# Optimization experiments

Measured on AMD Instinct MI355X. Metric: run time of the kernel, lower is better.

## Reference

```python
import jax, jax.numpy as jnp
import numpy as np
import math

DIM = 1024
HEADS = 16
WINDOW = 256  # window_size; also used as block size (band covers 3 blocks)


def _rope(x):
    # canonical half-split RoPE over the FULL feature dim (as the module applies
    # it before the head split), base 10000
    b, s, d = x.shape
    half = d // 2
    inv_freq = 1.0 / (10000.0 ** (jnp.arange(half, dtype=jnp.float32) / half))
    ang = jnp.arange(s, dtype=jnp.float32)[:, None] * inv_freq[None, :]  # [s, half]
    cos, sin = jnp.cos(ang), jnp.sin(ang)
    x1, x2 = x[..., :half], x[..., half:]
    return jnp.concatenate([x1 * cos - x2 * sin, x1 * sin + x2 * cos], axis=-1)


def setup_inputs() -> dict:
    key = jax.random.key(0)
    ks = jax.random.split(key, 8)
    d = DIM
    q = jax.random.normal(ks[0], (2, 4096, d), dtype=jnp.float32)
    k = jax.random.normal(ks[1], (2, 4096, d), dtype=jnp.float32)
    v = jax.random.normal(ks[2], (2, 4096, d), dtype=jnp.float32)
    wq = jax.random.normal(ks[3], (d, d), dtype=jnp.float32) * 0.02
    wk = jax.random.normal(ks[4], (d, d), dtype=jnp.float32) * 0.02
    wv = jax.random.normal(ks[5], (d, d), dtype=jnp.float32) * 0.02
    wo_w = jax.random.normal(ks[6], (d, d), dtype=jnp.float32) * 0.02
    wo_b = jnp.zeros((d,), dtype=jnp.float32)
    return {"q": q, "k": k, "v": v, "wq": wq, "wk": wk, "wv": wv,
            "wo_w": wo_w, "wo_b": wo_b}


def reference(q, k, v, wq, wk, wv, wo_w, wo_b):
    b, s, d = q.shape
    h, W = HEADS, WINDOW
    dk = d // h
    B = W                      # block size == window -> band of 3 blocks
    nb = s // B

    # projections (torch Linear: x @ W^T), then RoPE over the full dim
    qp = _rope(jnp.einsum('bsd,ed->bse', q, wq))
    kp = _rope(jnp.einsum('bsd,ed->bse', k, wk))
    vp = jnp.einsum('bsd,ed->bse', v, wv)

    # split heads -> [b, h, s, dk]
    qh = qp.reshape(b, s, h, dk).transpose(0, 2, 1, 3)
    kh = kp.reshape(b, s, h, dk).transpose(0, 2, 1, 3)
    vh = vp.reshape(b, s, h, dk).transpose(0, 2, 1, 3)

    # pad keys/values by one block on each side, gather 3-block bands
    kpad = jnp.pad(kh, ((0, 0), (0, 0), (B, B), (0, 0)))
    vpad = jnp.pad(vh, ((0, 0), (0, 0), (B, B), (0, 0)))
    kblk = kpad.reshape(b, h, nb + 2, B, dk)
    vblk = vpad.reshape(b, h, nb + 2, B, dk)
    kband = jnp.concatenate([kblk[:, :, i:i + nb] for i in range(3)], axis=3)  # [b,h,nb,3B,dk]
    vband = jnp.concatenate([vblk[:, :, i:i + nb] for i in range(3)], axis=3)

    qb = qh.reshape(b, h, nb, B, dk)
    # NOTE: original multiplies by sqrt(dim_k) (not divides) -- kept faithfully
    scores = jnp.einsum('bhnqd,bhnkd->bhnqk', qb, kband) * math.sqrt(dk)

    # band mask: key global pos = (n-1)*B + ki, query global pos = n*B + qi
    n_idx = jnp.arange(nb)[:, None, None]
    qi = jnp.arange(B)[None, :, None]
    ki = jnp.arange(3 * B)[None, None, :]
    kpos = (n_idx - 1) * B + ki
    rel = ki - B - qi  # key_pos - query_pos
    valid = (rel >= -W) & (rel <= W) & (kpos >= 0) & (kpos < s)  # [nb,B,3B]

    neg = jnp.asarray(jnp.finfo(scores.dtype).min, scores.dtype)
    scores = jnp.where(valid[None, None], scores, neg)
    attn = jax.nn.softmax(scores, axis=-1)

    out = jnp.einsum('bhnqk,bhnkd->bhnqd', attn, vband)
    out = out.reshape(b, h, s, dk).transpose(0, 2, 1, 3).reshape(b, s, d)
    return jnp.einsum('bsd,ed->bse', out, wo_w) + wo_b
```

## Files before the change

kernel.cpp:

```cpp
#include <hip/hip_runtime.h>


typedef __attribute__((ext_vector_type(8))) short short8v;
typedef __attribute__((ext_vector_type(4))) float float4v;
typedef __attribute__((ext_vector_type(8))) _Float16 half8v;

#define MFMA_BF16(A_, B_, C_) __builtin_amdgcn_mfma_f32_16x16x32_bf16((A_), (B_), (C_), 0, 0, 0)
#define MFMA_F16(A_, B_, C_)  __builtin_amdgcn_mfma_f32_16x16x32_f16((A_), (B_), (C_), 0, 0, 0)

#define VMW_(n) asm volatile("s_waitcnt vmcnt(" #n ")" ::: "memory")
#define VMW(n) VMW_(n)
#define LGKM0 asm volatile("s_waitcnt lgkmcnt(0)" ::: "memory")
#define BARF do { __builtin_amdgcn_s_barrier(); asm volatile("" ::: "memory"); } while (0)
#define FENCE asm volatile("" ::: "memory")

__device__ __forceinline__ void split_rn(float x, short& h, short& l) {
    unsigned int u = __float_as_uint(x);
    u += 0x7fffu + ((u >> 16) & 1u);
    unsigned int hb = u & 0xffff0000u;
    h = (short)(hb >> 16);
    float lo = x - __uint_as_float(hb);
    l = (short)(__float_as_uint(lo) >> 16);
}

__device__ __forceinline__ void dma16(const void* g, void* l) {
    __builtin_amdgcn_global_load_lds(
        (__attribute__((address_space(1))) void*)g,
        (__attribute__((address_space(3))) void*)l, 16, 0, 0);
}

__global__ __launch_bounds__(256) void prep_k(
    const float* __restrict__ wq, const float* __restrict__ wk,
    const float* __restrict__ wv, unsigned short* __restrict__ scr)
{
    const int M1 = 1 << 20;
    unsigned int tid = blockIdx.x * 256 + threadIdx.x;
    if (tid < (unsigned)M1) {
        short h, l; split_rn(wq[tid], h, l);
        scr[tid] = (unsigned short)h;
        scr[M1 + tid] = (unsigned short)l;
    } else if (tid < (unsigned)(2 * M1)) {
        unsigned int i = tid - M1;
        short h, l; split_rn(wk[i], h, l);
        scr[2 * M1 + i] = (unsigned short)h;
        scr[3 * M1 + i] = (unsigned short)l;
    } else {
        unsigned int i = tid - 2 * M1;
        scr[4 * M1 + i] = __builtin_bit_cast(unsigned short, (_Float16)wv[i]);
    }
}

__global__ __launch_bounds__(512, 2) void gemm_qk2(
    const float* __restrict__ A0, const short* __restrict__ Bh0,
    const short* __restrict__ Bl0, float* __restrict__ C0,
    const float* __restrict__ A1, const short* __restrict__ Bh1,
    const short* __restrict__ Bl1, float* __restrict__ C1)
{
    __shared__ __align__(16) short S[2 * 32768];

    const int bid = blockIdx.x;
    const int cid = ((bid & 7) << 5) | (bid >> 3);
    const int z   = cid >> 7;
    const int rem = cid & 127;
    const int bm  = (rem >> 2) << 8;
    const int bn  = (rem & 3) << 8;

    const float* Ap  = z ? A1  : A0;
    const short* Bhp = z ? Bh1 : Bh0;
    const short* Blp = z ? Bl1 : Bl0;
    float*       Cp  = z ? C1  : C0;

    const int t = threadIdx.x;
    const int wave = t >> 6, lane = t & 63;
    const int c16 = lane & 15, quad = lane >> 4;
    const int wm = (wave >> 2) << 7;
    const int wn = (wave & 3) << 6;

    const int ar = t >> 1;
    const int ah16 = (t & 1) << 4;
    const int fA = (ar & 3) ^ ((ar >> 2) & 3);
    const int swA0 = ((((t & 1) << 1) | 0) ^ fA) << 3;
    const int swA1 = ((((t & 1) << 1) | 1) ^ fA) << 3;

    const int br  = lane >> 2;
    const int fsl = (((lane & 3) ^ ((br & 3) ^ ((br >> 2) & 3))) << 3);

    const int frd = ((quad ^ ((c16 & 3) ^ ((c16 >> 2) & 3))) << 3);

    float4v acc[8][4];
#pragma unroll
    for (int i = 0; i < 8; i++)
#pragma unroll
        for (int j = 0; j < 4; j++) acc[i][j] = (float4v){0.f, 0.f, 0.f, 0.f};

#define STAGE_B(pp, kk)                                                          \
    do {                                                                         \
        const size_t rb = (size_t)(bn + (wave << 5) + br) * 1024 + (kk) + fsl;   \
        short* dh = S + (pp) * 32768 + 16384 + (wave << 10);                     \
        short* dl = dh + 8192;                                                   \
        dma16(Bhp + rb,             dh);                                         \
        dma16(Bhp + rb + 16 * 1024, dh + 512);                                   \
        dma16(Blp + rb,             dl);                                         \
        dma16(Blp + rb + 16 * 1024, dl + 512);                                   \
    } while (0)

#define SPLIT_WRITE(sp_)                                                         \
    do {                                                                         \
        short8v h0, l0, h1, l1;                                                  \
        _Pragma("unroll")                                                        \
        for (int jj = 0; jj < 4; jj++) {                                         \
            short hh, ll;                                                        \
            split_rn(ap0[jj], hh, ll); h0[jj] = hh;     l0[jj] = ll;             \
            split_rn(ap1[jj], hh, ll); h0[jj + 4] = hh; l0[jj + 4] = ll;         \
            split_rn(ap2[jj], hh, ll); h1[jj] = hh;     l1[jj] = ll;             \
            split_rn(ap3[jj], hh, ll); h1[jj + 4] = hh; l1[jj + 4] = ll;         \
        }                                                                        \
        short* abase = (sp_) + ar * 32;                                          \
        *(short8v*)(abase + swA0) = h0;                                          \
        *(short8v*)(abase + swA1) = h1;                                          \
        *(short8v*)(abase + 8192 + swA0) = l0;                                   \
        *(short8v*)(abase + 8192 + swA1) = l1;                                   \
    } while (0)

#define MFMA_CLUSTER(AARR, BARR)                                                 \
    do {                                                                         \
        __builtin_amdgcn_s_setprio(1);                                           \
        _Pragma("unroll")                                                        \
        for (int i = 0; i < 8; i++)                                              \
            _Pragma("unroll")                                                    \
            for (int j = 0; j < 4; j++)                                          \
                acc[i][j] = MFMA_BF16(AARR[i & 7], BARR[j & 3], acc[i][j]);      \
        __builtin_amdgcn_s_setprio(0);                                           \
    } while (0)

    const float* arow = Ap + (size_t)(bm + ar) * 1024 + ah16;
    float4v ap0 = *(const float4v*)(arow + 0);
    float4v ap1 = *(const float4v*)(arow + 4);
    float4v ap2 = *(const float4v*)(arow + 8);
    float4v ap3 = *(const float4v*)(arow + 12);
    FENCE;
    STAGE_B(0, 0);
    VMW(4);
    SPLIT_WRITE(S);
    FENCE;
    ap0 = *(const float4v*)(arow + 32);
    ap1 = *(const float4v*)(arow + 36);
    ap2 = *(const float4v*)(arow + 40);
    ap3 = *(const float4v*)(arow + 44);
    LGKM0;

    int kb = 0;
#pragma unroll 1
    for (int tt = 0; tt < 31; ++tt, kb += 32) {
        short* sp = S + (tt & 1) * 32768;
        short* sn = S + ((tt & 1) ^ 1) * 32768;

        STAGE_B((tt & 1) ^ 1, kb + 32);
        VMW(8);
        BARF;

        short8v ahv[8], bhv[4];
#pragma unroll
        for (int i = 0; i < 8; i++)
            ahv[i] = *(const short8v*)(sp + (wm + i * 16 + c16) * 32 + frd);
#pragma unroll
        for (int j = 0; j < 4; j++)
            bhv[j] = *(const short8v*)(sp + 16384 + (wn + j * 16 + c16) * 32 + frd);
        MFMA_CLUSTER(ahv, bhv);

        {
            short8v blv[4];
#pragma unroll
            for (int j = 0; j < 4; j++)
                blv[j] = *(const short8v*)(sp + 24576 + (wn + j * 16 + c16) * 32 + frd);
            MFMA_CLUSTER(ahv, blv);
        }

        VMW(4);
        SPLIT_WRITE(sn);
        FENCE;
        {
            int kn = kb + 64;
            if (kn >= 1024) kn = 0;
            ap0 = *(const float4v*)(arow + kn);
            ap1 = *(const float4v*)(arow + kn + 4);
            ap2 = *(const float4v*)(arow + kn + 8);
            ap3 = *(const float4v*)(arow + kn + 12);
        }

        {
            short8v alv[8];
#pragma unroll
            for (int i = 0; i < 8; i++)
                alv[i] = *(const short8v*)(sp + 8192 + (wm + i * 16 + c16) * 32 + frd);
            MFMA_CLUSTER(alv, bhv);
        }
        LGKM0;
        BARF;
    }

    {
        short* sp = S + 32768;
        VMW(4);
        BARF;
        short8v ahv[8], bhv[4];
#pragma unroll
        for (int i = 0; i < 8; i++)
            ahv[i] = *(const short8v*)(sp + (wm + i * 16 + c16) * 32 + frd);
#pragma unroll
        for (int j = 0; j < 4; j++)
            bhv[j] = *(const short8v*)(sp + 16384 + (wn + j * 16 + c16) * 32 + frd);
        MFMA_CLUSTER(ahv, bhv);
        {
            short8v blv[4];
#pragma unroll
            for (int j = 0; j < 4; j++)
                blv[j] = *(const short8v*)(sp + 24576 + (wn + j * 16 + c16) * 32 + frd);
            MFMA_CLUSTER(ahv, blv);
        }
        {
            short8v alv[8];
#pragma unroll
            for (int i = 0; i < 8; i++)
                alv[i] = *(const short8v*)(sp + 8192 + (wm + i * 16 + c16) * 32 + frd);
            MFMA_CLUSTER(alv, bhv);
        }
    }

#undef STAGE_B
#undef SPLIT_WRITE
#undef MFMA_CLUSTER

#pragma unroll
    for (int i = 0; i < 8; i++) {
        const size_t gr0 = (size_t)(bm + wm + i * 16 + quad * 4);
#pragma unroll
        for (int j = 0; j < 4; j++) {
            const int gc = bn + wn + j * 16 + c16;
#pragma unroll
            for (int r = 0; r < 4; r++)
                Cp[(gr0 + r) * 1024 + gc] = acc[i][j][r];
        }
    }
}

template <int ADMA, int OMODE>
__global__ __launch_bounds__(256, 2) void gemm16_2(
    const void* __restrict__ Ap, const void* __restrict__ Bp,
    void* __restrict__ Cp, const float* __restrict__ bias)
{
    __shared__ __align__(16) short S[2 * 8192];

    const int bid = blockIdx.x;
    const int cid = ((bid & 7) << 6) | (bid >> 3);
    const int bm  = (cid >> 3) << 7;
    const int bn  = (cid & 7) << 7;

    const _Float16* Dp = (const _Float16*)(ADMA ? Ap : Bp);
    const float*    Fp = (const float*)   (ADMA ? Bp : Ap);
    const int bd   = ADMA ? bm : bn;
    const int bf   = ADMA ? bn : bm;
    const int dOff = ADMA ? 0 : 4096;
    const int fOff = ADMA ? 4096 : 0;

    const int t = threadIdx.x;
    const int wave = t >> 6, lane = t & 63;
    const int c16 = lane & 15, quad = lane >> 4;
    const int wm = (wave >> 1) << 6;
    const int wn = (wave & 1) << 6;
    const int lr = t >> 2;
    const int lc = (t & 3) << 3;

    float4v acc[4][4];
#pragma unroll
    for (int i = 0; i < 4; i++)
#pragma unroll
        for (int j = 0; j < 4; j++) acc[i][j] = (float4v){0.f, 0.f, 0.f, 0.f};

    float4v f00, f01, f10, f11;

#define STAGE_DMA(pp, kk)                                                        \
    do {                                                                         \
        dma16(Dp + (size_t)(bd + lr) * 1024 + (kk) + lc,                         \
              S + (pp) * 8192 + dOff + (wave << 9));                             \
        dma16(Dp + (size_t)(bd + 64 + lr) * 1024 + (kk) + lc,                    \
              S + (pp) * 8192 + dOff + 2048 + (wave << 9));                      \
    } while (0)

#define LOAD_F(kk)                                                               \
    do {                                                                         \
        FENCE;                                                                   \
        const float* s0_ = Fp + (size_t)(bf + lr) * 1024 + (kk) + lc;            \
        const float* s1_ = Fp + (size_t)(bf + 64 + lr) * 1024 + (kk) + lc;       \
        f00 = *(const float4v*)s0_;  f01 = *(const float4v*)(s0_ + 4);           \
        f10 = *(const float4v*)s1_;  f11 = *(const float4v*)(s1_ + 4);           \
    } while (0)

#define CVT_WRITE(pp)                                                            \
    do {                                                                         \
        half8v h0_, h1_;                                                         \
        _Pragma("unroll")                                                        \
        for (int jj = 0; jj < 4; jj++) {                                         \
            h0_[jj] = (_Float16)f00[jj]; h0_[jj + 4] = (_Float16)f01[jj];        \
            h1_[jj] = (_Float16)f10[jj]; h1_[jj + 4] = (_Float16)f11[jj];        \
        }                                                                        \
        *(half8v*)(S + (pp) * 8192 + fOff + lr * 32 + lc) = h0_;                 \
        *(half8v*)(S + (pp) * 8192 + fOff + (64 + lr) * 32 + lc) = h1_;          \
    } while (0)

    LOAD_F(0);
    STAGE_DMA(0, 0);
    VMW(2);
    CVT_WRITE(0);
    LOAD_F(32);
    LGKM0;

#pragma unroll 1
    for (int tt = 0; tt < 31; ++tt) {
        const int kb = tt << 5;
        const int p = tt & 1;
        short* sp = S + p * 8192;

        STAGE_DMA(p ^ 1, kb + 32);
        VMW(6);
        BARF;

        half8v ah[4], bh[4];
#pragma unroll
        for (int i = 0; i < 4; i++)
            ah[i] = *(const half8v*)(sp + (wm + i * 16 + c16) * 32 + quad * 8);
#pragma unroll
        for (int j = 0; j < 4; j++)
            bh[j] = *(const half8v*)(sp + 4096 + (wn + j * 16 + c16) * 32 + quad * 8);
        __builtin_amdgcn_s_setprio(1);
#pragma unroll
        for (int i = 0; i < 4; i++)
#pragma unroll
            for (int j = 0; j < 4; j++)
                acc[i][j] = MFMA_F16(ah[i], bh[j], acc[i][j]);
        __builtin_amdgcn_s_setprio(0);

        VMW(2);
        CVT_WRITE(p ^ 1);
        {
            int kn = kb + 64;
            if (kn >= 1024) kn = 0;
            LOAD_F(kn);
        }
        LGKM0;
        BARF;
    }

    {
        short* sp = S + 8192;
        VMW(4);
        BARF;
        half8v ah[4], bh[4];
#pragma unroll
        for (int i = 0; i < 4; i++)
            ah[i] = *(const half8v*)(sp + (wm + i * 16 + c16) * 32 + quad * 8);
#pragma unroll
        for (int j = 0; j < 4; j++)
            bh[j] = *(const half8v*)(sp + 4096 + (wn + j * 16 + c16) * 32 + quad * 8);
        __builtin_amdgcn_s_setprio(1);
#pragma unroll
        for (int i = 0; i < 4; i++)
#pragma unroll
            for (int j = 0; j < 4; j++)
                acc[i][j] = MFMA_F16(ah[i], bh[j], acc[i][j]);
        __builtin_amdgcn_s_setprio(0);
    }

#undef STAGE_DMA
#undef LOAD_F
#undef CVT_WRITE

#pragma unroll
    for (int i = 0; i < 4; i++)
#pragma unroll
        for (int j = 0; j < 4; j++)
#pragma unroll
            for (int r = 0; r < 4; r++) {
                int gr = bm + wm + i * 16 + quad * 4 + r;
                int gc = bn + wn + j * 16 + c16;
                float vv = acc[i][j][r];
                if (OMODE == 0) {
                    ((unsigned short*)Cp)[((size_t)(gc << 1) + (gr >> 12)) * 4096 + (gr & 4095)] =
                        __builtin_bit_cast(unsigned short, (_Float16)vv);
                } else {
                    ((float*)Cp)[(size_t)gr * 1024 + gc] = vv + bias[gc];
                }
            }
}

__global__ __launch_bounds__(256) void rope_pack(float* __restrict__ QP, float* __restrict__ KP)
{
    int sp = blockIdx.x;
    int t = threadIdx.x;
    float* rows[4] = { QP + ((size_t)sp << 10), QP + ((size_t)(4096 + sp) << 10),
                       KP + ((size_t)sp << 10), KP + ((size_t)(4096 + sp) << 10) };

    float c[2], sn[2];
    float x1[4][2], x2[4][2];
#pragma unroll
    for (int p = 0; p < 2; p++) {
        int j = t + p * 256;
        float freq = __expf(-0.017988946f * (float)j);
        float ang = (float)sp * freq;
        sincosf(ang, &sn[p], &c[p]);
#pragma unroll
        for (int r = 0; r < 4; r++) {
            x1[r][p] = rows[r][j];
            x2[r][p] = rows[r][j + 512];
        }
    }
    __syncthreads();
#pragma unroll
    for (int r = 0; r < 4; r++) {
        unsigned short* u = (unsigned short*)rows[r];
        const float sc8 = (r < 2) ? 8.0f : 1.0f;
#pragma unroll
        for (int p = 0; p < 2; p++) {
            int j = t + p * 256;
            float y1 = (x1[r][p] * c[p] - x2[r][p] * sn[p]) * sc8;
            float y2 = (x1[r][p] * sn[p] + x2[r][p] * c[p]) * sc8;
            short h1, l1, h2, l2;
            split_rn(y1, h1, l1);
            split_rn(y2, h2, l2);
            u[j] = (unsigned short)h1;
            u[j + 512] = (unsigned short)h2;
            u[1024 + j] = (unsigned short)l1;
            u[1024 + j + 512] = (unsigned short)l2;
        }
    }
}

__global__ __launch_bounds__(512, 4) void attn_k(
    const unsigned short* __restrict__ QHL, const unsigned short* __restrict__ KHL,
    const unsigned short* __restrict__ VT, unsigned short* __restrict__ AO)
{
    const int S = 4096;
    const float NEG = -1e30f;
    const float PSC = 512.0f;
    const int bq = blockIdx.x, h = blockIdx.y, b = blockIdx.z;
    const int t = threadIdx.x;
    const int wave = t >> 6, lane = t & 63;
    const int col = lane & 15, quad = lane >> 4;
    const int qg = (bq << 7) + (wave << 4);

    __shared__ __align__(16) short Khs[2][64 * 64];
    __shared__ __align__(16) short Kls[2][64 * 64];
    __shared__ __align__(16) short Vs [2][64 * 64];
    __shared__ __align__(16) short Ps[8][16 * 72];
    short* myP = &Ps[wave][0];

    const int rg = lane >> 3;
    const int ch = (((lane & 7) ^ rg) << 3);
    const int srow = (wave << 3) + rg;

    const unsigned short* kbase = KHL + ((size_t)(b * S + srow) << 11) + h * 64 + ch;
    const unsigned short* vbase = VT + ((size_t)((h * 64 + srow) << 1) + b) * S + ch;

#define STAGE(pp, kk)                                          \
    do {                                                       \
        const unsigned short* kr = kbase + ((size_t)(kk) << 11); \
        dma16(kr,        &Khs[pp][wave << 9]);                 \
        dma16(kr + 1024, &Kls[pp][wave << 9]);                 \
        dma16(vbase + (kk), &Vs[pp][wave << 9]);               \
    } while (0)

    short8v qh[2], ql[2];
    {
        const unsigned short* qr = QHL + ((size_t)(b * S + qg + col) << 11) + h * 64 + quad * 8;
        qh[0] = *(const short8v*)(qr);
        qh[1] = *(const short8v*)(qr + 32);
        ql[0] = *(const short8v*)(qr + 1024);
        ql[1] = *(const short8v*)(qr + 1024 + 32);
    }

    float mrun[4], lrun[4], psum[4];
    float4v O[4];
#pragma unroll
    for (int r = 0; r < 4; r++) { mrun[r] = NEG; lrun[r] = 0.f; }
#pragma unroll
    for (int t4 = 0; t4 < 4; t4++) O[t4] = (float4v){0.f, 0.f, 0.f, 0.f};

    const int blk0 = bq << 7;
    const int kstart = (blk0 - 256 > 0) ? (blk0 - 256) : 0;
    const int kend = (blk0 + 384 < S) ? (blk0 + 384) : S;
    const int nt = (kend - kstart) >> 6;

    STAGE(0, kstart);

#pragma unroll 1
    for (int it = 0; it < nt; ++it) {
        const int kb = kstart + (it << 6);
        const int p = it & 1;
        if (it + 1 < nt) { STAGE(p ^ 1, kb + 64); VMW(3); }
        else             { VMW(0); }
        BARF;

        const short* KHp = &Khs[p][0];
        const short* KLp = &Kls[p][0];
        float4v sv[4];
        __builtin_amdgcn_s_setprio(1);
#pragma unroll
        for (int c = 0; c < 4; c++) {
            const int row = c * 16 + col;
            const int c0 = ((quad ^ (col & 7)) << 3);
            const int c1 = (((quad + 4) ^ (col & 7)) << 3);
            const short* kro = KHp + (row << 6);
            const short* klo = KLp + (row << 6);
            short8v kh0 = *(const short8v*)(kro + c0);
            short8v kh1 = *(const short8v*)(kro + c1);
            short8v kl0 = *(const short8v*)(klo + c0);
            short8v kl1 = *(const short8v*)(klo + c1);
            float4v sc = (float4v){0.f, 0.f, 0.f, 0.f};
            sc = MFMA_BF16(qh[0], kh0, sc);
            sc = MFMA_BF16(qh[1], kh1, sc);
            sc = MFMA_BF16(qh[0], kl0, sc);
            sc = MFMA_BF16(qh[1], kl1, sc);
            sc = MFMA_BF16(ql[0], kh0, sc);
            sc = MFMA_BF16(ql[1], kh1, sc);
            sv[c] = sc;
        }
        __builtin_amdgcn_s_setprio(0);

        const bool masked = (kb < blk0 - 128) || (kb > blk0 + 192);
        float mx[4];
        if (masked) {
#pragma unroll
            for (int r = 0; r < 4; r++) {
                int qrow = qg + quad * 4 + r;
                float m = NEG;
#pragma unroll
                for (int c = 0; c < 4; c++) {
                    int key = kb + c * 16 + col;
                    float vv = (key >= qrow - 256 && key <= qrow + 256) ? sv[c][r] : NEG;
                    sv[c][r] = vv;
                    m = fmaxf(m, vv);
                }
                mx[r] = m;
            }
        } else {
#pragma unroll
            for (int r = 0; r < 4; r++)
                mx[r] = fmaxf(fmaxf(sv[0][r], sv[1][r]), fmaxf(sv[2][r], sv[3][r]));
        }
#pragma unroll
        for (int st = 1; st < 16; st <<= 1)
#pragma unroll
            for (int r = 0; r < 4; r++) mx[r] = fmaxf(mx[r], __shfl_xor(mx[r], st, 64));

#pragma unroll
        for (int r = 0; r < 4; r++) {
            if (mx[r] > mrun[r]) {
                float al = __expf(mrun[r] - mx[r]);
                mrun[r] = mx[r];
                lrun[r] *= al;
#pragma unroll
                for (int t4 = 0; t4 < 4; t4++) O[t4][r] *= al;
            }
            float mn = mrun[r];
            float ps = 0.f;
#pragma unroll
            for (int c = 0; c < 4; c++) {
                float pv = __expf(sv[c][r] - mn);
                ps += pv;
                myP[(quad * 4 + r) * 72 + c * 16 + col] =
                    __builtin_bit_cast(short, (_Float16)(pv * PSC));
            }
            psum[r] = ps;
        }
#pragma unroll
        for (int st = 1; st < 16; st <<= 1)
#pragma unroll
            for (int r = 0; r < 4; r++) psum[r] += __shfl_xor(psum[r], st, 64);
#pragma unroll
        for (int r = 0; r < 4; r++) lrun[r] += psum[r];

        const short* Vp = &Vs[p][0];
        __builtin_amdgcn_s_setprio(1);
#pragma unroll
        for (int kf = 0; kf < 2; kf++) {
            half8v pa = *(const half8v*)(myP + col * 72 + kf * 32 + quad * 8);
#pragma unroll
            for (int t4 = 0; t4 < 4; t4++) {
                const int vrow = t4 * 16 + col;
                const int vc = ((((kf << 2) + quad) ^ (col & 7)) << 3);
                half8v vb = *(const half8v*)(Vp + (vrow << 6) + vc);
                O[t4] = MFMA_F16(pa, vb, O[t4]);
            }
        }
        __builtin_amdgcn_s_setprio(0);

        BARF;
    }
#undef STAGE

#pragma unroll
    for (int r = 0; r < 4; r++) {
        float inv = (lrun[r] > 0.f) ? (1.0f / (lrun[r] * PSC)) : 0.f;
        unsigned short* orow = AO + (size_t)(b * S + qg + quad * 4 + r) * 1024 + h * 64;
#pragma unroll
        for (int t4 = 0; t4 < 4; t4++)
            orow[t4 * 16 + col] = __builtin_bit_cast(unsigned short, (_Float16)(O[t4][r] * inv));
    }
}

extern "C" void kernel_launch(void* const* d_in, const int* in_sizes, int n_in,
                              void* d_out, int out_size, void* d_ws, size_t ws_size,
                              hipStream_t stream) {
    const float* q   = (const float*)d_in[0];
    const float* k   = (const float*)d_in[1];
    const float* v   = (const float*)d_in[2];
    const float* wq  = (const float*)d_in[3];
    const float* wk  = (const float*)d_in[4];
    const float* wv  = (const float*)d_in[5];
    const float* wo  = (const float*)d_in[6];
    const float* wob = (const float*)d_in[7];

    float* QP = (float*)d_ws;
    float* KP = QP + (size_t)8192 * 1024;
    unsigned short* VT = (unsigned short*)(KP + (size_t)8192 * 1024);
    unsigned short* AO = VT + (size_t)8192 * 1024;

    unsigned short* scr = (unsigned short*)d_out;
    const int M1 = 1 << 20;
    const short* wqh = (const short*)(scr);
    const short* wql = (const short*)(scr + M1);
    const short* wkh = (const short*)(scr + 2 * M1);
    const short* wkl = (const short*)(scr + 3 * M1);
    const void*  wv16 = (const void*)(scr + 4 * M1);

    prep_k<<<12288, 256, 0, stream>>>(wq, wk, wv, scr);
    gemm_qk2<<<dim3(256), 512, 0, stream>>>(q, wqh, wql, QP, k, wkh, wkl, KP);
    rope_pack<<<4096, 256, 0, stream>>>(QP, KP);
    gemm16_2<0, 0><<<512, 256, 0, stream>>>(v, wv16, (void*)VT, nullptr);
    attn_k<<<dim3(32, 16, 2), 512, 0, stream>>>((const unsigned short*)QP,
                                                (const unsigned short*)KP, VT, AO);
    gemm16_2<1, 1><<<512, 256, 0, stream>>>(AO, wo, d_out, wob);
}
```

Baseline: 393.6 us.

## Use 32x32 MFMA in projection GEMM and DPP reductions with exp2 softmax

The split-bf16 projection GEMM moves from 16x16x32 MFMA tiles to 32x32x16 tiles, so each wave issues fewer, larger matrix instructions and reads fewer LDS fragments per FLOP, at the cost of a changed accumulator layout and store pattern. In the attention kernel, the shuffle-based 16-lane max and sum reductions become DPP row operations. The softmax switches from __expf to exp2f by folding log2(e) into the Q scale (8 becomes 11.54). The fixed PSC multiply is replaced by a -9 offset in the exponent, which scales P by 512 before fp16 conversion. This removes per-element multiplies but relies on exp2 scaling to stay within fp16 range.

```diff
diff --git a/kernel.cpp b/kernel.cpp
--- a/kernel.cpp
+++ b/kernel.cpp
@@ -3,9 +3,11 @@
 
 typedef __attribute__((ext_vector_type(8))) short short8v;
 typedef __attribute__((ext_vector_type(4))) float float4v;
+typedef __attribute__((ext_vector_type(16))) float float16v;
 typedef __attribute__((ext_vector_type(8))) _Float16 half8v;
 
 #define MFMA_BF16(A_, B_, C_) __builtin_amdgcn_mfma_f32_16x16x32_bf16((A_), (B_), (C_), 0, 0, 0)
+#define MFMA_BF16_32(A_, B_, C_) __builtin_amdgcn_mfma_f32_32x32x16_bf16((A_), (B_), (C_), 0, 0, 0)
 #define MFMA_F16(A_, B_, C_)  __builtin_amdgcn_mfma_f32_16x16x32_f16((A_), (B_), (C_), 0, 0, 0)
 
 #define VMW_(n) asm volatile("s_waitcnt vmcnt(" #n ")" ::: "memory")
@@ -27,6 +29,26 @@
     __builtin_amdgcn_global_load_lds(
         (__attribute__((address_space(1))) void*)g,
         (__attribute__((address_space(3))) void*)l, 16, 0, 0);
+}
+
+template <int CTRL>
+__device__ __forceinline__ float dppf(float x) {
+    return __builtin_bit_cast(float,
+        __builtin_amdgcn_update_dpp(0, __builtin_bit_cast(int, x), CTRL, 0xF, 0xF, true));
+}
+__device__ __forceinline__ float red16_max(float x) {
+    x = fmaxf(x, dppf<0x128>(x));
+    x = fmaxf(x, dppf<0x124>(x));
+    x = fmaxf(x, dppf<0x4E>(x));
+    x = fmaxf(x, dppf<0xB1>(x));
+    return x;
+}
+__device__ __forceinline__ float red16_sum(float x) {
+    x += dppf<0x128>(x);
+    x += dppf<0x124>(x);
+    x += dppf<0x4E>(x);
+    x += dppf<0xB1>(x);
+    return x;
 }
 
 __global__ __launch_bounds__(256) void prep_k(
@@ -72,7 +94,7 @@
 
     const int t = threadIdx.x;
     const int wave = t >> 6, lane = t & 63;
-    const int c16 = lane & 15, quad = lane >> 4;
+    const int l31 = lane & 31, l5 = lane >> 5;
     const int wm = (wave >> 2) << 7;
     const int wn = (wave & 3) << 6;
 
@@ -85,13 +107,15 @@
     const int br  = lane >> 2;
     const int fsl = (((lane & 3) ^ ((br & 3) ^ ((br >> 2) & 3))) << 3);
 
-    const int frd = ((quad ^ ((c16 & 3) ^ ((c16 >> 2) & 3))) << 3);
-
-    float4v acc[8][4];
-#pragma unroll
-    for (int i = 0; i < 8; i++)
-#pragma unroll
-        for (int j = 0; j < 4; j++) acc[i][j] = (float4v){0.f, 0.f, 0.f, 0.f};
+    const int fL = (l31 & 3) ^ ((l31 >> 2) & 3);
+
+    float16v acc[4][2];
+#pragma unroll
+    for (int i = 0; i < 4; i++)
+#pragma unroll
+        for (int j = 0; j < 2; j++)
+#pragma unroll
+            for (int v = 0; v < 16; v++) acc[i][j][v] = 0.f;
 
 #define STAGE_B(pp, kk)                                                          \
     do {                                                                         \
@@ -122,14 +146,33 @@
         *(short8v*)(abase + 8192 + swA1) = l1;                                   \
     } while (0)
 
+#define LOAD_A8(ARR, base_)                                                      \
+    _Pragma("unroll")                                                            \
+    for (int ms = 0; ms < 4; ms++)                                               \
+        _Pragma("unroll")                                                        \
+        for (int ks = 0; ks < 2; ks++)                                           \
+            ARR[ms * 2 + ks] = *(const short8v*)((base_) +                       \
+                (wm + ms * 32 + l31) * 32 + ((((ks << 1) + l5) ^ fL) << 3))
+
+#define LOAD_B4(ARR, base_)                                                      \
+    _Pragma("unroll")                                                            \
+    for (int ns = 0; ns < 2; ns++)                                               \
+        _Pragma("unroll")                                                        \
+        for (int ks = 0; ks < 2; ks++)                                           \
+            ARR[ns * 2 + ks] = *(const short8v*)((base_) +                       \
+                (wn + ns * 32 + l31) * 32 + ((((ks << 1) + l5) ^ fL) << 3))
+
 #define MFMA_CLUSTER(AARR, BARR)                                                 \
     do {                                                                         \
         __builtin_amdgcn_s_setprio(1);                                           \
         _Pragma("unroll")                                                        \
-        for (int i = 0; i < 8; i++)                                              \
+        for (int ks = 0; ks < 2; ks++)                                           \
             _Pragma("unroll")                                                    \
-            for (int j = 0; j < 4; j++)                                          \
-                acc[i][j] = MFMA_BF16(AARR[i & 7], BARR[j & 3], acc[i][j]);      \
+            for (int ms = 0; ms < 4; ms++)                                       \
+                _Pragma("unroll")                                                \
+                for (int ns = 0; ns < 2; ns++)                                   \
+                    acc[ms][ns] = MFMA_BF16_32(AARR[ms * 2 + ks],                \
+                                               BARR[ns * 2 + ks], acc[ms][ns]);  \
         __builtin_amdgcn_s_setprio(0);                                           \
     } while (0)
 
@@ -160,19 +203,13 @@
         BARF;
 
         short8v ahv[8], bhv[4];
-#pragma unroll
-        for (int i = 0; i < 8; i++)
-            ahv[i] = *(const short8v*)(sp + (wm + i * 16 + c16) * 32 + frd);
-#pragma unroll
-        for (int j = 0; j < 4; j++)
-            bhv[j] = *(const short8v*)(sp + 16384 + (wn + j * 16 + c16) * 32 + frd);
+        LOAD_A8(ahv, sp);
+        LOAD_B4(bhv, sp + 16384);
         MFMA_CLUSTER(ahv, bhv);
 
         {
             short8v blv[4];
-#pragma unroll
-            for (int j = 0; j < 4; j++)
-                blv[j] = *(const short8v*)(sp + 24576 + (wn + j * 16 + c16) * 32 + frd);
+            LOAD_B4(blv, sp + 24576);
             MFMA_CLUSTER(ahv, blv);
         }
 
@@ -190,9 +227,7 @@
 
         {
             short8v alv[8];
-#pragma unroll
-            for (int i = 0; i < 8; i++)
-                alv[i] = *(const short8v*)(sp + 8192 + (wm + i * 16 + c16) * 32 + frd);
+            LOAD_A8(alv, sp + 8192);
             MFMA_CLUSTER(alv, bhv);
         }
         LGKM0;
@@ -204,44 +239,37 @@
         VMW(4);
         BARF;
         short8v ahv[8], bhv[4];
-#pragma unroll
-        for (int i = 0; i < 8; i++)
-            ahv[i] = *(const short8v*)(sp + (wm + i * 16 + c16) * 32 + frd);
-#pragma unroll
-        for (int j = 0; j < 4; j++)
-            bhv[j] = *(const short8v*)(sp + 16384 + (wn + j * 16 + c16) * 32 + frd);
+        LOAD_A8(ahv, sp);
+        LOAD_B4(bhv, sp + 16384);
         MFMA_CLUSTER(ahv, bhv);
         {
             short8v blv[4];
-#pragma unroll
-            for (int j = 0; j < 4; j++)
-                blv[j] = *(const short8v*)(sp + 24576 + (wn + j * 16 + c16) * 32 + frd);
+            LOAD_B4(blv, sp + 24576);
             MFMA_CLUSTER(ahv, blv);
         }
         {
             short8v alv[8];
-#pragma unroll
-            for (int i = 0; i < 8; i++)
-                alv[i] = *(const short8v*)(sp + 8192 + (wm + i * 16 + c16) * 32 + frd);
+            LOAD_A8(alv, sp + 8192);
             MFMA_CLUSTER(alv, bhv);
         }
     }
 
 #undef STAGE_B
 #undef SPLIT_WRITE
+#undef LOAD_A8
+#undef LOAD_B4
 #undef MFMA_CLUSTER
 
 #pragma unroll
-    for (int i = 0; i < 8; i++) {
-        const size_t gr0 = (size_t)(bm + wm + i * 16 + quad * 4);
-#pragma unroll
-        for (int j = 0; j < 4; j++) {
-            const int gc = bn + wn + j * 16 + c16;
-#pragma unroll
-            for (int r = 0; r < 4; r++)
-                Cp[(gr0 + r) * 1024 + gc] = acc[i][j][r];
-        }
-    }
+    for (int ms = 0; ms < 4; ms++)
+#pragma unroll
+        for (int ns = 0; ns < 2; ns++)
+#pragma unroll
+            for (int v = 0; v < 16; v++) {
+                int grow = bm + wm + ms * 32 + 4 * l5 + (v & 3) + 8 * (v >> 2);
+                int gcol = bn + wn + ns * 32 + l31;
+                Cp[(size_t)grow * 1024 + gcol] = acc[ms][ns][v];
+            }
 }
 
 template <int ADMA, int OMODE>
@@ -418,7 +446,7 @@
 #pragma unroll
     for (int r = 0; r < 4; r++) {
         unsigned short* u = (unsigned short*)rows[r];
-        const float sc8 = (r < 2) ? 8.0f : 1.0f;
+        const float sc8 = (r < 2) ? 11.541560f : 1.0f;
 #pragma unroll
         for (int p = 0; p < 2; p++) {
             int j = t + p * 256;
@@ -441,7 +469,6 @@
 {
     const int S = 4096;
     const float NEG = -1e30f;
-    const float PSC = 512.0f;
     const int bq = blockIdx.x, h = blockIdx.y, b = blockIdx.z;
     const int t = threadIdx.x;
     const int wave = t >> 6, lane = t & 63;
@@ -478,7 +505,7 @@
         ql[1] = *(const short8v*)(qr + 1024 + 32);
     }
 
-    float mrun[4], lrun[4], psum[4];
+    float mrun[4], lrun[4];
     float4v O[4];
 #pragma unroll
     for (int r = 0; r < 4; r++) { mrun[r] = NEG; lrun[r] = 0.f; }
@@ -548,36 +575,28 @@
                 mx[r] = fmaxf(fmaxf(sv[0][r], sv[1][r]), fmaxf(sv[2][r], sv[3][r]));
         }
 #pragma unroll
-        for (int st = 1; st < 16; st <<= 1)
-#pragma unroll
-            for (int r = 0; r < 4; r++) mx[r] = fmaxf(mx[r], __shfl_xor(mx[r], st, 64));
+        for (int r = 0; r < 4; r++) mx[r] = red16_max(mx[r]);
 
 #pragma unroll
         for (int r = 0; r < 4; r++) {
             if (mx[r] > mrun[r]) {
-                float al = __expf(mrun[r] - mx[r]);
+                float al = exp2f(mrun[r] - mx[r]);
                 mrun[r] = mx[r];
                 lrun[r] *= al;
 #pragma unroll
                 for (int t4 = 0; t4 < 4; t4++) O[t4][r] *= al;
             }
-            float mn = mrun[r];
+            float mn9 = mrun[r] - 9.0f;
             float ps = 0.f;
 #pragma unroll
             for (int c = 0; c < 4; c++) {
-                float pv = __expf(sv[c][r] - mn);
+                float pv = exp2f(sv[c][r] - mn9);
                 ps += pv;
                 myP[(quad * 4 + r) * 72 + c * 16 + col] =
-                    __builtin_bit_cast(short, (_Float16)(pv * PSC));
+                    __builtin_bit_cast(short, (_Float16)pv);
             }
-            psum[r] = ps;
-        }
-#pragma unroll
-        for (int st = 1; st < 16; st <<= 1)
-#pragma unroll
-            for (int r = 0; r < 4; r++) psum[r] += __shfl_xor(psum[r], st, 64);
-#pragma unroll
-        for (int r = 0; r < 4; r++) lrun[r] += psum[r];
+            lrun[r] += red16_sum(ps);
+        }
 
         const short* Vp = &Vs[p][0];
         __builtin_amdgcn_s_setprio(1);
@@ -600,7 +619,7 @@
 
 #pragma unroll
     for (int r = 0; r < 4; r++) {
-        float inv = (lrun[r] > 0.f) ? (1.0f / (lrun[r] * PSC)) : 0.f;
+        float inv = (lrun[r] > 0.f) ? (1.0f / lrun[r]) : 0.f;
         unsigned short* orow = AO + (size_t)(b * S + qg + quad * 4 + r) * 1024 + h * 64;
 #pragma unroll
         for (int t4 = 0; t4 < 4; t4++)
```

New measurement: 403.5 us. 1.03x slower.
